# Performance work log

Measured on AMD Instinct MI355X. Metric: run time of the kernel, lower is better.

## Reference

```python
import jax, jax.numpy as jnp
import numpy as np

EMB = 2048
NH = 16
HD = EMB // NH  # 128

def setup_inputs() -> dict:
    key = jax.random.key(0)
    kx, kw1, kw2 = jax.random.split(key, 3)
    T = 4096
    x = jax.random.normal(kx, (T, EMB), dtype=jnp.float32)
    lim_in = 1.0 / np.sqrt(EMB)
    # input_proj: Linear(EMB, 3*EMB, use_bias=False), weight shape (out, in)
    W_in = jax.random.uniform(kw1, (3 * EMB, EMB), minval=-lim_in, maxval=lim_in, dtype=jnp.float32)
    W_out = jax.random.uniform(kw2, (EMB, EMB), minval=-lim_in, maxval=lim_in, dtype=jnp.float32)
    return {"x": x, "W_in": W_in, "W_out": W_out}

def reference(x, W_in, W_out):
    T = x.shape[0]
    norm = 1.0 / np.sqrt(HD)
    qkv = x @ W_in.T                         # [T, 3E]
    Q, K, V = jnp.split(qkv, 3, axis=-1)     # each [T, E]
    Q = Q.reshape(T, NH, HD).transpose(1, 0, 2)  # [nh, T, hd]
    K = K.reshape(T, NH, HD).transpose(1, 0, 2)
    V = V.reshape(T, NH, HD).transpose(1, 0, 2)
    A = jnp.einsum('htd,hsd->hts', Q, K) * norm  # [nh, T, T]
    mask = jnp.tri(T, dtype=bool)                # causal: keep lower triangle
    A = jnp.where(mask, A, -jnp.inf)
    P = jax.nn.softmax(A, axis=-1)
    y = jnp.einsum('hts,hsd->htd', P, V)         # [nh, T, hd]
    y = y.transpose(1, 0, 2).reshape(T, EMB)     # concat heads
    return y @ W_out.T
```

## Files before the change

### kernel.cpp

```cpp
#include <hip/hip_runtime.h>
#include <hip/hip_bf16.h>
#include <cstddef>


typedef __attribute__((ext_vector_type(8))) short short8;
typedef __attribute__((ext_vector_type(4))) float f32x4;

#define MFMA16(a, b, c) __builtin_amdgcn_mfma_f32_16x16x32_bf16((a), (b), (c), 0, 0, 0)

#define GLOAD_LDS16(gptr, lptr)                                                          \
  __builtin_amdgcn_global_load_lds((const __attribute__((address_space(1))) void*)(gptr), \
                                   (__attribute__((address_space(3))) void*)(lptr), 16, 0, 0)

#define PSWZ(q) ((((q) & 7) ^ ((q) >> 3)) << 3)

__device__ __forceinline__ short f2bf(float f) {
  __hip_bfloat16 h = __float2bfloat16(f);
  return *reinterpret_cast<short*>(&h);
}

__device__ __forceinline__ void storeC(float* p, float v) { *p = v; }
__device__ __forceinline__ void storeC(short* p, float v) { *p = f2bf(v); }

__global__ void cvt_all(const float* __restrict__ x, short* __restrict__ xb, long nx,
                        const float* __restrict__ w1, short* __restrict__ w1b, long nw1,
                        const float* __restrict__ w2, short* __restrict__ w2b, long nw2,
                        float qs, long qn) {
  long i = ((long)blockIdx.x * 256 + threadIdx.x) * 8;
  const float* in; short* out; float s = 1.0f;
  if (i < nx) {
    in = x + i; out = xb + i;
  } else if ((i -= nx) < nw1) {
    in = w1 + i; out = w1b + i; if (i < qn) s = qs;
  } else if ((i -= nw1) < nw2) {
    in = w2 + i; out = w2b + i;
  } else {
    return;
  }
  f32x4 a = *(const f32x4*)(in);
  f32x4 b = *(const f32x4*)(in + 4);
  short8 o;
  o[0] = f2bf(a[0] * s); o[1] = f2bf(a[1] * s); o[2] = f2bf(a[2] * s); o[3] = f2bf(a[3] * s);
  o[4] = f2bf(b[0] * s); o[5] = f2bf(b[1] * s); o[6] = f2bf(b[2] * s); o[7] = f2bf(b[3] * s);
  *(short8*)(out) = o;
}

template <typename CT>
__global__ __launch_bounds__(256, 4)
void gemm_bt(const short* __restrict__ A, const short* __restrict__ B,
             CT* __restrict__ C, int M, int N, int K) {
  __shared__ short As[128 * 64];
  __shared__ short Bs[128 * 64];
  const int tid = threadIdx.x;
  const int wave = tid >> 6, lane = tid & 63;
  const int g = lane >> 4, fr = lane & 15;
  const int wr = (wave >> 1) * 64, wc = (wave & 1) * 64;
  const int bm = blockIdx.y * 128, bn = blockIdx.x * 128;

  f32x4 acc[4][4] = {};

  for (int k0 = 0; k0 < K; k0 += 64) {
    __syncthreads();
#pragma unroll
    for (int i = 0; i < 4; ++i) {
      int Ci = i * 256 + tid;
      int row = Ci >> 3, c = Ci & 7;
      int sc = c ^ (row & 7);
      GLOAD_LDS16(A + (size_t)(bm + row) * K + k0 + sc * 8, As + Ci * 8);
      GLOAD_LDS16(B + (size_t)(bn + row) * K + k0 + sc * 8, Bs + Ci * 8);
    }
    __syncthreads();

#pragma unroll
    for (int kk = 0; kk < 2; ++kk) {
      short8 af[4], bfr[4];
#pragma unroll
      for (int m = 0; m < 4; ++m) {
        int row = wr + m * 16 + fr;
        int off = (kk * 32 + g * 8) ^ ((row & 7) * 8);
        af[m] = *(const short8*)(As + row * 64 + off);
      }
#pragma unroll
      for (int n = 0; n < 4; ++n) {
        int row = wc + n * 16 + fr;
        int off = (kk * 32 + g * 8) ^ ((row & 7) * 8);
        bfr[n] = *(const short8*)(Bs + row * 64 + off);
      }
#pragma unroll
      for (int m = 0; m < 4; ++m)
#pragma unroll
        for (int n = 0; n < 4; ++n)
          acc[m][n] = MFMA16(af[m], bfr[n], acc[m][n]);
    }
  }

#pragma unroll
  for (int m = 0; m < 4; ++m) {
#pragma unroll
    for (int r = 0; r < 4; ++r) {
      size_t row = (size_t)(bm + wr + m * 16 + g * 4 + r);
      CT* cp = C + row * N + bn + wc + fr;
#pragma unroll
      for (int n = 0; n < 4; ++n)
        storeC(cp + n * 16, acc[m][n][r]);
    }
  }
}

__global__ __launch_bounds__(256, 4)
void vtrans(const short* __restrict__ qkv, short* __restrict__ vtg) {
  __shared__ short L[128 * 64];
  const int tid = threadIdx.x;
  const int tb = blockIdx.x * 64;
  const int h = blockIdx.y;
#pragma unroll
  for (int i = 0; i < 4; ++i) {
    int Ci = i * 256 + tid, tok = Ci >> 4, c = Ci & 15, f0 = c * 8;
    short8 v = *(const short8*)(qkv + (size_t)(tb + tok) * 6144 + 4096 + h * 128 + f0);
#pragma unroll
    for (int j = 0; j < 8; ++j) {
      int f = f0 + j;
      L[f * 64 + (tok ^ ((((f & 7) ^ ((f >> 3) & 7)) << 3)))] = v[j];
    }
  }
  __syncthreads();
  const int f = tid >> 1, half = (tid & 1) * 32;
  const int s_in = ((f & 7) ^ ((f >> 3) & 7)) << 3;
  const int s_out = (f & 7) << 3;
#pragma unroll
  for (int j2 = 0; j2 < 4; ++j2) {
    int t0 = half + j2 * 8;
    short8 v = *(const short8*)(&L[f * 64 + (t0 ^ s_in)]);
    *(short8*)(vtg + (size_t)(h * 128 + f) * 4096 + tb + (t0 ^ s_out)) = v;
  }
}

__global__ __launch_bounds__(256, 2)
void attn_fwd(const short* __restrict__ qkv, const short* __restrict__ vtg,
              short* __restrict__ y) {
  __shared__ short Ks[2][64 * 128];
  __shared__ short Vt[128 * 64];
  __shared__ short Ps[4][32 * 64];
  const int tid = threadIdx.x;
  const int wave = tid >> 6, lane = tid & 63;
  const int g = lane >> 4, fr = lane & 15;

  const int wgid = blockIdx.x;
  const int xcd = wgid & 7, mid = (wgid >> 3) & 31, slot = wgid >> 8;
  const int h = (xcd << 1) | (mid & 1);
  const int xq = mid >> 1;
  const int x = slot ? xq : 31 - xq;
  const int qw = x * 128 + wave * 32;
  const int ntiles = 2 * x + 2;

  short* Pw = Ps[wave];

  short8 onesf;
#pragma unroll
  for (int j = 0; j < 8; ++j) onesf[j] = (short)0x3F80;

  short8 qf[2][4];
#pragma unroll
  for (int mi = 0; mi < 2; ++mi) {
    const short* Qp = qkv + (size_t)(qw + mi * 16 + fr) * 6144 + h * 128;
#pragma unroll
    for (int kk = 0; kk < 4; ++kk)
      qf[mi][kk] = *(const short8*)(Qp + kk * 32 + g * 8);
  }
  f32x4 oacc[2][8] = {};
  f32x4 lacc[2] = {};

#pragma unroll
  for (int i = 0; i < 4; ++i) {
    int Ci = i * 256 + tid, key = Ci >> 4, c = Ci & 15, sc = c ^ (key & 7);
    GLOAD_LDS16(qkv + (size_t)key * 6144 + 2048 + h * 128 + sc * 8, &Ks[0][Ci * 8]);
  }
#pragma unroll
  for (int i = 0; i < 4; ++i) {
    int Ci = i * 256 + tid, feat = Ci >> 3, ko = (Ci & 7) * 8;
    GLOAD_LDS16(vtg + (size_t)(h * 128 + feat) * 4096 + ko, &Vt[Ci * 8]);
  }
  __syncthreads();

#pragma unroll 1
  for (int t = 0; t < ntiles; ++t) {
    const int kv0 = t * 64;
    const int cur = t & 1;

    if (t > 0) {
#pragma unroll
      for (int i = 0; i < 4; ++i) {
        int Ci = i * 256 + tid, feat = Ci >> 3, ko = (Ci & 7) * 8;
        GLOAD_LDS16(vtg + (size_t)(h * 128 + feat) * 4096 + kv0 + ko, &Vt[Ci * 8]);
      }
    }
    if (t + 1 < ntiles) {
#pragma unroll
      for (int i = 0; i < 4; ++i) {
        int Ci = i * 256 + tid, key = Ci >> 4, c = Ci & 15, sc = c ^ (key & 7);
        GLOAD_LDS16(qkv + (size_t)(kv0 + 64 + key) * 6144 + 2048 + h * 128 + sc * 8,
                    &Ks[cur ^ 1][Ci * 8]);
      }
    }

    const bool active = (kv0 <= qw + 31);

    if (active) {
      f32x4 s[2][4] = {};
      __builtin_amdgcn_s_setprio(1);
#pragma unroll
      for (int nf = 0; nf < 4; ++nf) {
        const int key = nf * 16 + fr;
#pragma unroll
        for (int kk = 0; kk < 4; ++kk) {
          int off = (kk * 32 + g * 8) ^ ((key & 7) * 8);
          short8 kfrag = *(const short8*)(&Ks[cur][key * 128 + off]);
          s[0][nf] = MFMA16(qf[0][kk], kfrag, s[0][nf]);
          s[1][nf] = MFMA16(qf[1][kk], kfrag, s[1][nf]);
        }
      }
      __builtin_amdgcn_s_setprio(0);

      if (t >= ntiles - 2) {
#pragma unroll
        for (int mi = 0; mi < 2; ++mi)
#pragma unroll
          for (int nf = 0; nf < 4; ++nf) {
            const int keyg = kv0 + nf * 16 + fr;
#pragma unroll
            for (int r = 0; r < 4; ++r) {
              const int q2 = mi * 16 + g * 4 + r;
              float p = (keyg <= qw + q2) ? __builtin_amdgcn_exp2f(s[mi][nf][r]) : 0.f;
              Pw[q2 * 64 + ((nf * 16 + fr) ^ PSWZ(q2))] = f2bf(p);
            }
          }
      } else {
#pragma unroll
        for (int mi = 0; mi < 2; ++mi)
#pragma unroll
          for (int nf = 0; nf < 4; ++nf)
#pragma unroll
            for (int r = 0; r < 4; ++r) {
              const int q2 = mi * 16 + g * 4 + r;
              Pw[q2 * 64 + ((nf * 16 + fr) ^ PSWZ(q2))] =
                  f2bf(__builtin_amdgcn_exp2f(s[mi][nf][r]));
            }
      }
    }

    __syncthreads();

    if (active) {
      __builtin_amdgcn_s_setprio(1);
#pragma unroll
      for (int kk = 0; kk < 2; ++kk) {
        const int rb = kk * 32 + g * 8;
        short8 pf0 = *(const short8*)(&Pw[fr * 64 + (rb ^ PSWZ(fr))]);
        short8 pf1 = *(const short8*)(&Pw[(16 + fr) * 64 + (rb ^ PSWZ(16 + fr))]);
        lacc[0] = MFMA16(pf0, onesf, lacc[0]);
        lacc[1] = MFMA16(pf1, onesf, lacc[1]);
#pragma unroll
        for (int nf = 0; nf < 8; ++nf) {
          int f = nf * 16 + fr;
          short8 vf = *(const short8*)(&Vt[f * 64 + (rb ^ ((f & 7) * 8))]);
          oacc[0][nf] = MFMA16(pf0, vf, oacc[0][nf]);
          oacc[1][nf] = MFMA16(pf1, vf, oacc[1][nf]);
        }
      }
      __builtin_amdgcn_s_setprio(0);
    }

    __syncthreads();
  }

#pragma unroll
  for (int mi = 0; mi < 2; ++mi)
#pragma unroll
    for (int r = 0; r < 4; ++r) {
      float inv = 1.0f / lacc[mi][r];
      size_t row = (size_t)(qw + mi * 16 + g * 4 + r);
#pragma unroll
      for (int nf = 0; nf < 8; ++nf)
        y[row * 2048 + h * 128 + nf * 16 + fr] = f2bf(oacc[mi][nf][r] * inv);
    }
}

extern "C" void kernel_launch(void* const* d_in, const int* in_sizes, int n_in,
                              void* d_out, int out_size, void* d_ws, size_t ws_size,
                              hipStream_t stream) {
  const float* x    = (const float*)d_in[0];
  const float* Win  = (const float*)d_in[1];
  const float* Wout = (const float*)d_in[2];
  float* out = (float*)d_out;

  char* ws = (char*)d_ws;
  short* xb    = (short*)(ws);
  short* yb    = (short*)(ws);
  short* Winb  = (short*)(ws + 16777216);
  short* vtg   = (short*)(ws + 16777216);
  short* Woutb = (short*)(ws + 41943040);
  short* qkv   = (short*)(ws + 50331648);

  const float qscale = 0.08838834764831845f * 1.4426950408889634f;

  cvt_all<<<12288, 256, 0, stream>>>(x, xb, 8388608L,
                                     Win, Winb, 12582912L,
                                     Wout, Woutb, 4194304L,
                                     qscale, 4194304L);

  gemm_bt<short><<<dim3(48, 32), 256, 0, stream>>>(xb, Winb, qkv, 4096, 6144, 2048);

  vtrans<<<dim3(64, 16), 256, 0, stream>>>(qkv, vtg);

  attn_fwd<<<512, 256, 0, stream>>>(qkv, vtg, yb);

  gemm_bt<float><<<dim3(16, 32), 256, 0, stream>>>(yb, Woutb, out, 4096, 2048, 2048);
}
```

Before: 281.8 us.

## Split long causal attention rows across two workgroups with a merge kernel

For the longer half of query blocks (x>=16), attention is split along the KV axis into two workgroups, each writing unnormalized bf16 partial outputs and row sums to workspace. A new merge kernel adds the partials and normalizes them. The aim is to balance per-workgroup work under the causal mask and raise the grid from 512 to 768 workgroups for better CU occupancy. The cost is an extra launch, extra global traffic for the partials, and bf16 rounding of the partial sums. The merge is correct only because the kernel uses no running max, so the two halves share the same scale.

```diff
diff --git a/kernel.cpp b/kernel.cpp
--- a/kernel.cpp
+++ b/kernel.cpp
@@ -17,6 +17,12 @@
 __device__ __forceinline__ short f2bf(float f) {
   __hip_bfloat16 h = __float2bfloat16(f);
   return *reinterpret_cast<short*>(&h);
+}
+
+__device__ __forceinline__ float bf2f(short s) {
+  union { unsigned u; float f; } v;
+  v.u = ((unsigned)(unsigned short)s) << 16;
+  return v.f;
 }
 
 __device__ __forceinline__ void storeC(float* p, float v) { *p = v; }
@@ -137,7 +143,8 @@
 
 __global__ __launch_bounds__(256, 2)
 void attn_fwd(const short* __restrict__ qkv, const short* __restrict__ vtg,
-              short* __restrict__ y) {
+              short* __restrict__ y, short* __restrict__ Opart,
+              float* __restrict__ lpart) {
   __shared__ short Ks[2][64 * 128];
   __shared__ short Vt[128 * 64];
   __shared__ short Ps[4][32 * 64];
@@ -146,12 +153,21 @@
   const int g = lane >> 4, fr = lane & 15;
 
   const int wgid = blockIdx.x;
-  const int xcd = wgid & 7, mid = (wgid >> 3) & 31, slot = wgid >> 8;
-  const int h = (xcd << 1) | (mid & 1);
-  const int xq = mid >> 1;
-  const int x = slot ? xq : 31 - xq;
+  const int xcd = wgid & 7;
+  const int rest = wgid >> 3;
+  const int h = (xcd << 1) | (rest & 1);
+  const int u = rest >> 1;
+  int x, t0, t1, half;
+  bool whole;
+  if (u < 32) {
+    x = 16 + (u >> 1); half = u & 1; whole = false;
+    t0 = half * (x + 1); t1 = (half + 1) * (x + 1);
+  } else {
+    x = 47 - u; half = 0; whole = true;
+    t0 = 0; t1 = 2 * x + 2;
+  }
   const int qw = x * 128 + wave * 32;
-  const int ntiles = 2 * x + 2;
+  const int ntg = 2 * x + 2;
 
   short* Pw = Ps[wave];
 
@@ -173,28 +189,29 @@
 #pragma unroll
   for (int i = 0; i < 4; ++i) {
     int Ci = i * 256 + tid, key = Ci >> 4, c = Ci & 15, sc = c ^ (key & 7);
-    GLOAD_LDS16(qkv + (size_t)key * 6144 + 2048 + h * 128 + sc * 8, &Ks[0][Ci * 8]);
+    GLOAD_LDS16(qkv + (size_t)(t0 * 64 + key) * 6144 + 2048 + h * 128 + sc * 8,
+                &Ks[0][Ci * 8]);
   }
 #pragma unroll
   for (int i = 0; i < 4; ++i) {
     int Ci = i * 256 + tid, feat = Ci >> 3, ko = (Ci & 7) * 8;
-    GLOAD_LDS16(vtg + (size_t)(h * 128 + feat) * 4096 + ko, &Vt[Ci * 8]);
+    GLOAD_LDS16(vtg + (size_t)(h * 128 + feat) * 4096 + t0 * 64 + ko, &Vt[Ci * 8]);
   }
   __syncthreads();
 
 #pragma unroll 1
-  for (int t = 0; t < ntiles; ++t) {
+  for (int t = t0; t < t1; ++t) {
     const int kv0 = t * 64;
-    const int cur = t & 1;
-
-    if (t > 0) {
+    const int cur = (t - t0) & 1;
+
+    if (t > t0) {
 #pragma unroll
       for (int i = 0; i < 4; ++i) {
         int Ci = i * 256 + tid, feat = Ci >> 3, ko = (Ci & 7) * 8;
         GLOAD_LDS16(vtg + (size_t)(h * 128 + feat) * 4096 + kv0 + ko, &Vt[Ci * 8]);
       }
     }
-    if (t + 1 < ntiles) {
+    if (t + 1 < t1) {
 #pragma unroll
       for (int i = 0; i < 4; ++i) {
         int Ci = i * 256 + tid, key = Ci >> 4, c = Ci & 15, sc = c ^ (key & 7);
@@ -221,7 +238,7 @@
       }
       __builtin_amdgcn_s_setprio(0);
 
-      if (t >= ntiles - 2) {
+      if (t >= ntg - 2) {
 #pragma unroll
         for (int mi = 0; mi < 2; ++mi)
 #pragma unroll
@@ -273,16 +290,54 @@
     __syncthreads();
   }
 
-#pragma unroll
-  for (int mi = 0; mi < 2; ++mi)
-#pragma unroll
-    for (int r = 0; r < 4; ++r) {
-      float inv = 1.0f / lacc[mi][r];
-      size_t row = (size_t)(qw + mi * 16 + g * 4 + r);
-#pragma unroll
-      for (int nf = 0; nf < 8; ++nf)
-        y[row * 2048 + h * 128 + nf * 16 + fr] = f2bf(oacc[mi][nf][r] * inv);
-    }
+  if (whole) {
+#pragma unroll
+    for (int mi = 0; mi < 2; ++mi)
+#pragma unroll
+      for (int r = 0; r < 4; ++r) {
+        float inv = 1.0f / lacc[mi][r];
+        size_t row = (size_t)(qw + mi * 16 + g * 4 + r);
+#pragma unroll
+        for (int nf = 0; nf < 8; ++nf)
+          y[row * 2048 + h * 128 + nf * 16 + fr] = f2bf(oacc[mi][nf][r] * inv);
+      }
+  } else {
+    const size_t pb = (((size_t)h * 16 + (x - 16)) * 2 + half);
+    const size_t ob = pb * 16384;
+#pragma unroll
+    for (int mi = 0; mi < 2; ++mi)
+#pragma unroll
+      for (int r = 0; r < 4; ++r) {
+        const int rowq = wave * 32 + mi * 16 + g * 4 + r;
+#pragma unroll
+        for (int nf = 0; nf < 8; ++nf)
+          Opart[ob + (size_t)rowq * 128 + nf * 16 + fr] = f2bf(oacc[mi][nf][r]);
+        if (fr == 0)
+          lpart[pb * 128 + rowq] = lacc[mi][r];
+      }
+  }
+}
+
+__global__ __launch_bounds__(256, 8)
+void attn_merge(const short* __restrict__ Opart, const float* __restrict__ lpart,
+                short* __restrict__ y) {
+  const int tid = threadIdx.x;
+  const int xp = blockIdx.x, h = blockIdx.y;
+  const size_t ob = (((size_t)h * 16 + xp) * 2) * 16384;
+  const float* lp = lpart + ((size_t)h * 16 + xp) * 2 * 128;
+#pragma unroll
+  for (int v = 0; v < 8; ++v) {
+    int idx = v * 2048 + tid * 8;
+    int r = idx >> 7, d = idx & 127;
+    short8 a = *(const short8*)(Opart + ob + idx);
+    short8 b = *(const short8*)(Opart + ob + 16384 + idx);
+    float inv = 1.0f / (lp[r] + lp[128 + r]);
+    short8 o;
+#pragma unroll
+    for (int j = 0; j < 8; ++j)
+      o[j] = f2bf((bf2f(a[j]) + bf2f(b[j])) * inv);
+    *(short8*)(y + (size_t)(2048 + xp * 128 + r) * 2048 + h * 128 + d) = o;
+  }
 }
 
 extern "C" void kernel_launch(void* const* d_in, const int* in_sizes, int n_in,
@@ -298,8 +353,10 @@
   short* yb    = (short*)(ws);
   short* Winb  = (short*)(ws + 16777216);
   short* vtg   = (short*)(ws + 16777216);
+  float* lpart = (float*)(ws + 33554432);
   short* Woutb = (short*)(ws + 41943040);
   short* qkv   = (short*)(ws + 50331648);
+  short* Opart = (short*)(ws + 100663296);
 
   const float qscale = 0.08838834764831845f * 1.4426950408889634f;
 
@@ -312,7 +369,9 @@
 
   vtrans<<<dim3(64, 16), 256, 0, stream>>>(qkv, vtg);
 
-  attn_fwd<<<512, 256, 0, stream>>>(qkv, vtg, yb);
+  attn_fwd<<<768, 256, 0, stream>>>(qkv, vtg, yb, Opart, lpart);
+
+  attn_merge<<<dim3(16, 16), 256, 0, stream>>>(Opart, lpart, yb);
 
   gemm_bt<float><<<dim3(16, 32), 256, 0, stream>>>(yb, Woutb, out, 4096, 2048, 2048);
 }
```

Measured after the change: 280.5 us (median of 2 runs). Within noise of the previous version (-0.5%).
